# Performance work log

Measured on AMD Instinct MI355X. Metric: run time of the kernel, lower is better.

## Reference

```python
import jax, jax.numpy as jnp
import numpy as np

B, H_IN, W_IN = 8192, 26, 26

def _conv(x, w, b):
    # NCHW conv, stride 1, padding 1 (as in OffConv2d: padding hardcoded to 1)
    y = jax.lax.conv_general_dilated(x, w, (1, 1), [(1, 1), (1, 1)],
                                     dimension_numbers=('NCHW', 'OIHW', 'NCHW'))
    return y + b[None, :, None, None]

def _grid_sample_bilinear_zeros(img, gx, gy):
    # img: (N,H,W), gx/gy: (N,H,W) normalized coords; matches torch grid_sample
    # mode='bilinear', padding_mode='zeros', align_corners=False
    N, H, W = img.shape
    ix = ((gx + 1.0) * W - 1.0) * 0.5
    iy = ((gy + 1.0) * H - 1.0) * 0.5
    x0 = jnp.floor(ix); y0 = jnp.floor(iy)
    x1 = x0 + 1.0;      y1 = y0 + 1.0
    wx1 = ix - x0; wx0 = 1.0 - wx1
    wy1 = iy - y0; wy0 = 1.0 - wy1
    bi = jnp.arange(N)[:, None, None]
    def gather(yy, xx):
        valid = (xx >= 0) & (xx < W) & (yy >= 0) & (yy < H)
        v = img[bi,
                jnp.clip(yy, 0, H - 1).astype(jnp.int32),
                jnp.clip(xx, 0, W - 1).astype(jnp.int32)]
        return jnp.where(valid, v, 0.0)
    return (gather(y0, x0) * wy0 * wx0 + gather(y0, x1) * wy0 * wx1 +
            gather(y1, x0) * wy1 * wx0 + gather(y1, x1) * wy1 * wx1)

def _off_conv(x, ws, bs, wx, bx, wy, by):
    s  = _conv(x, ws, bs)   # score  (B,C,H,W)
    gx = _conv(x, wx, bx)   # offset_x -> grid x coord
    gy = _conv(x, wy, by)   # offset_y -> grid y coord
    b, c, h, w = s.shape
    out = _grid_sample_bilinear_zeros(s.reshape(b * c, h, w),
                                      gx.reshape(b * c, h, w),
                                      gy.reshape(b * c, h, w))
    return out.reshape(b, c, h, w)

def _maxpool2(x):
    return jax.lax.reduce_window(x, -jnp.inf, jax.lax.max,
                                 (1, 1, 2, 2), (1, 1, 2, 2), 'VALID')

def setup_inputs() -> dict:
    key = jax.random.key(0)
    ks = jax.random.split(key, 20)
    r = lambda k, shp, s: (jax.random.normal(k, shp, dtype=jnp.float32) * s)
    inp = {
        'x':   r(ks[0], (B, H_IN, W_IN), 1.0),
        'w1s': r(ks[1], (6, 1, 5, 5), 0.2),  'b1s': r(ks[2], (6,), 0.1),
        'w1x': r(ks[3], (6, 1, 5, 5), 0.2),  'b1x': r(ks[4], (6,), 0.1),
        'w1y': r(ks[5], (6, 1, 5, 5), 0.2),  'b1y': r(ks[6], (6,), 0.1),
        'w2s': r(ks[7], (16, 6, 5, 5), 0.1), 'b2s': r(ks[8], (16,), 0.1),
        'w2x': r(ks[9], (16, 6, 5, 5), 0.1), 'b2x': r(ks[10], (16,), 0.1),
        'w2y': r(ks[11], (16, 6, 5, 5), 0.1),'b2y': r(ks[12], (16,), 0.1),
        'wf1': r(ks[13], (120, 400), 0.05),  'bf1': r(ks[14], (120,), 0.05),
        'wf2': r(ks[15], (84, 120), 0.05),   'bf2': r(ks[16], (84,), 0.05),
        'wf3': r(ks[17], (10, 84), 0.05),    'bf3': r(ks[18], (10,), 0.05),
    }
    return inp

def reference(x, w1s, b1s, w1x, b1x, w1y, b1y,
              w2s, b2s, w2x, b2x, w2y, b2y,
              wf1, bf1, wf2, bf2, wf3, bf3):
    h = x[:, None, :, :]                                   # (B,1,26,26)
    h = _maxpool2(jax.nn.relu(_off_conv(h, w1s, b1s, w1x, b1x, w1y, b1y)))  # (B,6,12,12)
    h = _maxpool2(jax.nn.relu(_off_conv(h, w2s, b2s, w2x, b2x, w2y, b2y)))  # (B,16,5,5)
    h = h.reshape(-1, 16 * 5 * 5)
    h = jax.nn.relu(h @ wf1.T + bf1)
    h = jax.nn.relu(h @ wf2.T + bf2)
    h = h @ wf3.T + bf3
    return jax.nn.softmax(h, axis=1)
```

## Files before the change

### kernel.cpp

```cpp
#include <hip/hip_runtime.h>
#include <math.h>

#define TPB 256

typedef float v2f __attribute__((ext_vector_type(2)));

__device__ __forceinline__ void pk_lo(v2f& acc, v2f ap, v2f w) {
    asm("v_pk_fma_f32 %0, %1, %2, %0 op_sel:[0,0,0] op_sel_hi:[0,1,1]"
        : "+v"(acc) : "v"(ap), "v"(w));
}
__device__ __forceinline__ void pk_hi(v2f& acc, v2f ap, v2f w) {
    asm("v_pk_fma_f32 %0, %1, %2, %0 op_sel:[1,0,0] op_sel_hi:[1,1,1]"
        : "+v"(acc) : "v"(ap), "v"(w));
}

#define OFF_WA_SX 0
#define OFF_WA_YY 300
#define OFF_WB_SX 464
#define OFF_WB_YY 5264
#define OFF_WF1T  7664
#define OFF_WF2T  55664
#define OFF_WF3T  65744
#define OFF_H1    66592
#define OFF_H2    7144480
#define WS_FLOATS 10421280ull
#define REQ_WS_BYTES (WS_FLOATS * 4ull)

__device__ __forceinline__ float bilin_zero(const float* __restrict__ img, int N,
                                            float gx, float gy) {
    float fx = (gx + 1.0f) * (0.5f * (float)N) - 0.5f;
    float fy = (gy + 1.0f) * (0.5f * (float)N) - 0.5f;
    float x0 = floorf(fx), y0 = floorf(fy);
    float wx1 = fx - x0, wy1 = fy - y0;
    float wx0 = 1.0f - wx1, wy0 = 1.0f - wy1;
    float x1 = x0 + 1.0f, y1 = y0 + 1.0f;
    float Nm1 = (float)(N - 1);
    int xi0 = (int)fminf(fmaxf(x0, 0.0f), Nm1);
    int yi0 = (int)fminf(fmaxf(y0, 0.0f), Nm1);
    int xi1 = (int)fminf(fmaxf(x1, 0.0f), Nm1);
    int yi1 = (int)fminf(fmaxf(y1, 0.0f), Nm1);
    bool vx0 = (x0 >= 0.0f) && (x0 < (float)N);
    bool vx1 = (x1 >= 0.0f) && (x1 < (float)N);
    bool vy0 = (y0 >= 0.0f) && (y0 < (float)N);
    bool vy1 = (y1 >= 0.0f) && (y1 < (float)N);
    float v00 = (vy0 && vx0) ? img[yi0 * N + xi0] : 0.0f;
    float v01 = (vy0 && vx1) ? img[yi0 * N + xi1] : 0.0f;
    float v10 = (vy1 && vx0) ? img[yi1 * N + xi0] : 0.0f;
    float v11 = (vy1 && vx1) ? img[yi1 * N + xi1] : 0.0f;
    return v00 * wy0 * wx0 + v01 * wy0 * wx1 + v10 * wy1 * wx0 + v11 * wy1 * wx1;
}

__global__ __launch_bounds__(TPB) void lenet_prep(
    const float* __restrict__ w1s, const float* __restrict__ w1x, const float* __restrict__ w1y,
    const float* __restrict__ w2s, const float* __restrict__ w2x, const float* __restrict__ w2y,
    const float* __restrict__ wf1, const float* __restrict__ wf2, const float* __restrict__ wf3,
    float* __restrict__ wsf)
{
    int g = blockIdx.x * TPB + threadIdx.x;
    int stride = gridDim.x * TPB;
    for (int i = g; i < 75; i += stride) {
        int cp = i / 25, t = i % 25;
        int cA = (2 * cp) * 25 + t, cB = (2 * cp + 1) * 25 + t;
        float* p = wsf + OFF_WA_SX + i * 4;
        p[0] = w1s[cA]; p[1] = w1x[cA]; p[2] = w1s[cB]; p[3] = w1x[cB];
        wsf[OFF_WA_YY + i * 2 + 0] = w1y[cA];
        wsf[OFF_WA_YY + i * 2 + 1] = w1y[cB];
    }
    for (int e = g; e < 1200; e += stride) {
        int cp = e / 150, rem = e % 150;
        int iA = cp * 150 + rem, iB = (cp + 8) * 150 + rem;
        float* pp = wsf + OFF_WB_SX + e * 4;
        pp[0] = w2s[iA]; pp[1] = w2s[iB]; pp[2] = w2x[iA]; pp[3] = w2x[iB];
        wsf[OFF_WB_YY + e * 2 + 0] = w2y[iA];
        wsf[OFF_WB_YY + e * 2 + 1] = w2y[iB];
    }
    for (int i = g; i < 48000; i += stride) { int k = i / 120, o = i % 120; wsf[OFF_WF1T + i] = wf1[o * 400 + k]; }
    for (int i = g; i < 10080; i += stride) { int k = i / 84,  o = i % 84;  wsf[OFF_WF2T + i] = wf2[o * 120 + k]; }
    for (int i = g; i < 840;   i += stride) { int k = i / 10,  o = i % 10;  wsf[OFF_WF3T + i] = wf3[o * 84 + k]; }
}

__global__ __launch_bounds__(TPB) void lenetA(
    const float* __restrict__ x, const float* __restrict__ wsf,
    const float* __restrict__ b1s, const float* __restrict__ b1x, const float* __restrict__ b1y,
    float* __restrict__ h1)
{
    __shared__ __align__(16) float xs_p[784];
    __shared__ __align__(16) float smap1[3456];

    const int tid = threadIdx.x, b = blockIdx.x;
    const float* xp = x + b * 676;
    for (int i = tid; i < 784; i += TPB) {
        int r = i / 28, c = i % 28;
        float v = 0.0f;
        if (r >= 1 && r <= 26 && c >= 1 && c <= 26) v = xp[(r - 1) * 26 + (c - 1)];
        xs_p[i] = v;
    }
    __syncthreads();

    const float4* wsx = (const float4*)(wsf + OFF_WA_SX);
    const v2f*    wyy = (const v2f*)   (wsf + OFF_WA_YY);

    float gxa[2][2][2][2], gya[2][2][2][2];
    #pragma unroll
    for (int it = 0; it < 2; ++it) {
        int idx = tid + it * TPB;
        if (idx < 432) {
            int cp = idx / 144, p = idx % 144;
            int py = p / 12, px = p % 12;
            v2f aw[6][3];
            #pragma unroll
            for (int r = 0; r < 6; ++r) {
                const v2f* rp = (const v2f*)&xs_p[(2 * py + r) * 28 + 2 * px];
                aw[r][0] = rp[0]; aw[r][1] = rp[1]; aw[r][2] = rp[2];
            }
            int c0 = 2 * cp, c1 = 2 * cp + 1;
            v2f a0[2][2], a1[2][2], ay[2][2];
            {
                v2f i0 = {b1s[c0], b1x[c0]};
                v2f i1 = {b1s[c1], b1x[c1]};
                v2f iy = {b1y[c0], b1y[c1]};
                #pragma unroll
                for (int dy = 0; dy < 2; ++dy)
                    #pragma unroll
                    for (int dx = 0; dx < 2; ++dx) { a0[dy][dx] = i0; a1[dy][dx] = i1; ay[dy][dx] = iy; }
            }
            const float4* wp  = wsx + cp * 25;
            const v2f*    wyp = wyy + cp * 25;
            #pragma unroll
            for (int ky = 0; ky < 5; ++ky)
                #pragma unroll
                for (int kx = 0; kx < 5; ++kx) {
                    float4 w4 = wp[ky * 5 + kx];
                    v2f wA = {w4.x, w4.y};
                    v2f wB = {w4.z, w4.w};
                    v2f wy = wyp[ky * 5 + kx];
                    #pragma unroll
                    for (int dy = 0; dy < 2; ++dy)
                        #pragma unroll
                        for (int dx = 0; dx < 2; ++dx) {
                            int rr = ky + dy, cc = kx + dx;
                            v2f ap = aw[rr][cc >> 1];
                            if ((cc & 1) == 0) {
                                pk_lo(a0[dy][dx], ap, wA);
                                pk_lo(a1[dy][dx], ap, wB);
                                pk_lo(ay[dy][dx], ap, wy);
                            } else {
                                pk_hi(a0[dy][dx], ap, wA);
                                pk_hi(a1[dy][dx], ap, wB);
                                pk_hi(ay[dy][dx], ap, wy);
                            }
                        }
                }
            {
                v2f r00 = {a0[0][0].x, a0[0][1].x};
                v2f r01 = {a0[1][0].x, a0[1][1].x};
                v2f r10 = {a1[0][0].x, a1[0][1].x};
                v2f r11 = {a1[1][0].x, a1[1][1].x};
                *(v2f*)&smap1[c0 * 576 + (2 * py) * 24 + 2 * px]     = r00;
                *(v2f*)&smap1[c0 * 576 + (2 * py + 1) * 24 + 2 * px] = r01;
                *(v2f*)&smap1[c1 * 576 + (2 * py) * 24 + 2 * px]     = r10;
                *(v2f*)&smap1[c1 * 576 + (2 * py + 1) * 24 + 2 * px] = r11;
            }
            #pragma unroll
            for (int dy = 0; dy < 2; ++dy)
                #pragma unroll
                for (int dx = 0; dx < 2; ++dx) {
                    gxa[it][0][dy][dx] = a0[dy][dx].y;  gya[it][0][dy][dx] = ay[dy][dx].x;
                    gxa[it][1][dy][dx] = a1[dy][dx].y;  gya[it][1][dy][dx] = ay[dy][dx].y;
                }
        }
    }
    __syncthreads();

    #pragma unroll
    for (int it = 0; it < 2; ++it) {
        int idx = tid + it * TPB;
        if (idx < 432) {
            int cp = idx / 144, p = idx % 144;
            #pragma unroll
            for (int ch = 0; ch < 2; ++ch) {
                int c = 2 * cp + ch;
                const float* smc = &smap1[c * 576];
                float mx = 0.0f;
                #pragma unroll
                for (int dy = 0; dy < 2; ++dy)
                    #pragma unroll
                    for (int dx = 0; dx < 2; ++dx)
                        mx = fmaxf(mx, bilin_zero(smc, 24, gxa[it][ch][dy][dx], gya[it][ch][dy][dx]));
                h1[b * 864 + c * 144 + p] = mx;
            }
        }
    }
}

__global__ __launch_bounds__(TPB, 5) void lenetB(
    const float* __restrict__ h1, const float* __restrict__ wsf,
    const float* __restrict__ b2s, const float* __restrict__ b2x, const float* __restrict__ b2y,
    float* __restrict__ h2)
{
    __shared__ __align__(16) float h1p[2][1176];
    __shared__ __align__(16) float wsm[4][2][2][100];

    const int tid = threadIdx.x, b = blockIdx.x;

    for (int i = tid; i < 2352; i += TPB) {
        int im = (i >= 1176) ? 1 : 0;
        int k = i - im * 1176;
        int ch = k / 196, pp = k % 196;
        int r = pp / 14, c = pp % 14;
        float v = 0.0f;
        if (r >= 1 && r <= 12 && c >= 1 && c <= 12)
            v = h1[(size_t)(2 * b + im) * 864 + ch * 144 + (r - 1) * 12 + (c - 1)];
        h1p[im][k] = v;
    }
    __syncthreads();

    const int lane = tid & 63;
    const int wvu  = __builtin_amdgcn_readfirstlane(tid >> 6);
    const int img  = lane >> 5;
    const int p    = lane & 31;
    const bool act = (p < 25);
    const int py = p / 5, px = p % 5;

    const float4* wsx = (const float4*)(wsf + OFF_WB_SX);
    const v2f*    wyy = (const v2f*)   (wsf + OFF_WB_YY);
    float* smw = &wsm[wvu][img][0][0];

    #pragma unroll
    for (int rep = 0; rep < 2; ++rep) {
        const int cp = wvu + 4 * rep;
        if (rep) {
            asm volatile("s_waitcnt lgkmcnt(0)" ::: "memory");
            __builtin_amdgcn_sched_barrier(0);
        }
        v2f as[2][2], ax[2][2], ay[2][2];
        if (act) {
            {
                v2f is = {b2s[cp], b2s[cp + 8]};
                v2f ix = {b2x[cp], b2x[cp + 8]};
                v2f iy = {b2y[cp], b2y[cp + 8]};
                #pragma unroll
                for (int dy = 0; dy < 2; ++dy)
                    #pragma unroll
                    for (int dx = 0; dx < 2; ++dx) { as[dy][dx] = is; ax[dy][dx] = ix; ay[dy][dx] = iy; }
            }
            #pragma unroll
            for (int i = 0; i < 6; ++i) {
                v2f aw[6][3];
                #pragma unroll
                for (int r = 0; r < 6; ++r) {
                    const v2f* rp = (const v2f*)&h1p[img][i * 196 + (2 * py + r) * 14 + 2 * px];
                    aw[r][0] = rp[0]; aw[r][1] = rp[1]; aw[r][2] = rp[2];
                }
                const float4* wt  = wsx + (cp * 6 + i) * 25;
                const v2f*    wyt = wyy + (cp * 6 + i) * 25;
                #pragma unroll
                for (int ky = 0; ky < 5; ++ky)
                    #pragma unroll
                    for (int kx = 0; kx < 5; ++kx) {
                        float4 w4 = wt[ky * 5 + kx];
                        v2f ws = {w4.x, w4.y};
                        v2f wx = {w4.z, w4.w};
                        v2f wy = wyt[ky * 5 + kx];
                        #pragma unroll
                        for (int dy = 0; dy < 2; ++dy)
                            #pragma unroll
                            for (int dx = 0; dx < 2; ++dx) {
                                int cc = kx + dx;
                                v2f ap = aw[ky + dy][cc >> 1];
                                if ((cc & 1) == 0) {
                                    pk_lo(as[dy][dx], ap, ws);
                                    pk_lo(ax[dy][dx], ap, wx);
                                    pk_lo(ay[dy][dx], ap, wy);
                                } else {
                                    pk_hi(as[dy][dx], ap, ws);
                                    pk_hi(ax[dy][dx], ap, wx);
                                    pk_hi(ay[dy][dx], ap, wy);
                                }
                            }
                    }
            }
            {
                int base0 = (2 * py) * 10 + 2 * px;
                int base1 = base0 + 10;
                *(v2f*)&smw[base0]       = (v2f){as[0][0].x, as[0][1].x};
                *(v2f*)&smw[base1]       = (v2f){as[1][0].x, as[1][1].x};
                *(v2f*)&smw[100 + base0] = (v2f){as[0][0].y, as[0][1].y};
                *(v2f*)&smw[100 + base1] = (v2f){as[1][0].y, as[1][1].y};
            }
        }
        asm volatile("s_waitcnt lgkmcnt(0)" ::: "memory");
        __builtin_amdgcn_sched_barrier(0);
        if (act) {
            #pragma unroll
            for (int slot = 0; slot < 2; ++slot) {
                int c = cp + slot * 8;
                const float* smc = &smw[slot * 100];
                float mx = 0.0f;
                #pragma unroll
                for (int dy = 0; dy < 2; ++dy)
                    #pragma unroll
                    for (int dx = 0; dx < 2; ++dx) {
                        float gx = slot ? ax[dy][dx].y : ax[dy][dx].x;
                        float gy = slot ? ay[dy][dx].y : ay[dy][dx].x;
                        mx = fmaxf(mx, bilin_zero(smc, 10, gx, gy));
                    }
                h2[(size_t)(2 * b + img) * 400 + c * 25 + p] = mx;
            }
        }
    }
}

__global__ __launch_bounds__(TPB) void lenetC(
    const float* __restrict__ h2, const float* __restrict__ wsf,
    const float* __restrict__ bf1, const float* __restrict__ bf2, const float* __restrict__ bf3,
    float* __restrict__ out)
{
    __shared__ __align__(16) float h2s[4][4][400];
    __shared__ float f1s[4][4][120];
    __shared__ float f2s[4][4][84];
    __shared__ float f3s[4][4][10];

    const int tid = threadIdx.x;
    const int w = tid >> 6, lane = tid & 63;
    const int img0 = blockIdx.x * 16 + w * 4;

    for (int j = 0; j < 4; ++j) {
        float4*       dst = (float4*)&h2s[w][j][0];
        const float4* src = (const float4*)&h2[(img0 + j) * 400];
        for (int k = lane; k < 100; k += 64) dst[k] = src[k];
    }
    __syncthreads();

    {
        const float* wf1T = wsf + OFF_WF1T;
        float acc1[4] = {0, 0, 0, 0}, acc2[4] = {0, 0, 0, 0};
        for (int k = 0; k < 400; ++k) {
            float wa = wf1T[k * 120 + lane];
            float wb = (lane < 56) ? wf1T[k * 120 + 64 + lane] : 0.0f;
            #pragma unroll
            for (int j = 0; j < 4; ++j) {
                float hv = h2s[w][j][k];
                acc1[j] = fmaf(hv, wa, acc1[j]);
                acc2[j] = fmaf(hv, wb, acc2[j]);
            }
        }
        float bb1 = bf1[lane];
        float bb2 = (lane < 56) ? bf1[64 + lane] : 0.0f;
        #pragma unroll
        for (int j = 0; j < 4; ++j) {
            f1s[w][j][lane] = fmaxf(acc1[j] + bb1, 0.0f);
            if (lane < 56) f1s[w][j][64 + lane] = fmaxf(acc2[j] + bb2, 0.0f);
        }
    }
    __syncthreads();

    {
        const float* wf2T = wsf + OFF_WF2T;
        float acc1[4], acc2[4];
        float bb1 = bf2[lane];
        float bb2 = (lane < 20) ? bf2[64 + lane] : 0.0f;
        #pragma unroll
        for (int j = 0; j < 4; ++j) { acc1[j] = bb1; acc2[j] = bb2; }
        for (int k = 0; k < 120; ++k) {
            float wa = wf2T[k * 84 + lane];
            float wb = (lane < 20) ? wf2T[k * 84 + 64 + lane] : 0.0f;
            #pragma unroll
            for (int j = 0; j < 4; ++j) {
                float hv = f1s[w][j][k];
                acc1[j] = fmaf(hv, wa, acc1[j]);
                acc2[j] = fmaf(hv, wb, acc2[j]);
            }
        }
        #pragma unroll
        for (int j = 0; j < 4; ++j) {
            f2s[w][j][lane] = fmaxf(acc1[j], 0.0f);
            if (lane < 20) f2s[w][j][64 + lane] = fmaxf(acc2[j], 0.0f);
        }
    }
    __syncthreads();

    if (lane < 10) {
        const float* wf3T = wsf + OFF_WF3T;
        float acc[4];
        float bb = bf3[lane];
        #pragma unroll
        for (int j = 0; j < 4; ++j) acc[j] = bb;
        for (int k = 0; k < 84; ++k) {
            float wv = wf3T[k * 10 + lane];
            #pragma unroll
            for (int j = 0; j < 4; ++j) acc[j] = fmaf(f2s[w][j][k], wv, acc[j]);
        }
        #pragma unroll
        for (int j = 0; j < 4; ++j) f3s[w][j][lane] = acc[j];
    }
    __syncthreads();

    if (lane < 40) {
        int j = lane / 10, c = lane % 10;
        float m = f3s[w][j][0];
        #pragma unroll
        for (int q = 1; q < 10; ++q) m = fmaxf(m, f3s[w][j][q]);
        float ssum = 0.0f;
        #pragma unroll
        for (int q = 0; q < 10; ++q) ssum += expf(f3s[w][j][q] - m);
        out[(img0 + j) * 10 + c] = expf(f3s[w][j][c] - m) / ssum;
    }
}

__global__ __launch_bounds__(TPB, 2) void lenet_off_fused(
    const float* __restrict__ x,
    const float* __restrict__ w1s, const float* __restrict__ b1s,
    const float* __restrict__ w1x, const float* __restrict__ b1x,
    const float* __restrict__ w1y, const float* __restrict__ b1y,
    const float* __restrict__ w2s, const float* __restrict__ b2s,
    const float* __restrict__ w2x, const float* __restrict__ b2x,
    const float* __restrict__ w2y, const float* __restrict__ b2y,
    const float* __restrict__ wf1, const float* __restrict__ bf1,
    const float* __restrict__ wf2, const float* __restrict__ bf2,
    const float* __restrict__ wf3, const float* __restrict__ bf3,
    float* __restrict__ out)
{
    __shared__ __align__(16) float  xs_p[784];
    __shared__ float4 w1i[150];
    __shared__ float4 b1i[6];
    __shared__ float4 w2i[2400];
    __shared__ float4 b2i[16];
    __shared__ __align__(16) float  smap1[3456];
    __shared__ __align__(16) float  h1p[1176];
    __shared__ __align__(16) float  smap2[1600];
    __shared__ __align__(16) float  h2[400];
    __shared__ __align__(16) float  f1[120];
    __shared__ __align__(16) float  f2[84];
    __shared__ float  f3[10];

    const int tid = threadIdx.x;
    const int b   = blockIdx.x;

    const float* xp = x + b * 676;
    for (int i = tid; i < 784; i += TPB) {
        int r = i / 28, c = i % 28;
        float v = 0.0f;
        if (r >= 1 && r <= 26 && c >= 1 && c <= 26) v = xp[(r - 1) * 26 + (c - 1)];
        xs_p[i] = v;
    }
    for (int i = tid; i < 150; i += TPB)
        w1i[i] = make_float4(w1s[i], w1x[i], w1y[i], 0.0f);
    if (tid < 6)  b1i[tid] = make_float4(b1s[tid], b1x[tid], b1y[tid], 0.0f);
    for (int i = tid; i < 2400; i += TPB)
        w2i[i] = make_float4(w2s[i], w2x[i], w2y[i], 0.0f);
    if (tid < 16) b2i[tid] = make_float4(b2s[tid], b2x[tid], b2y[tid], 0.0f);
    for (int i = tid; i < 1176; i += TPB) h1p[i] = 0.0f;
    __syncthreads();

    float gxr[4][2][2], gyr[4][2][2];
    #pragma unroll
    for (int it = 0; it < 4; ++it) {
        int idx = tid + it * TPB;
        if (idx < 864) {
            int c = idx / 144, p = idx % 144;
            int py = p / 12, px = p % 12;
            float a[6][6];
            #pragma unroll
            for (int r = 0; r < 6; ++r) {
                const float2* rp = (const float2*)&xs_p[(2 * py + r) * 28 + 2 * px];
                float2 v0 = rp[0], v1 = rp[1], v2 = rp[2];
                a[r][0] = v0.x; a[r][1] = v0.y; a[r][2] = v1.x;
                a[r][3] = v1.y; a[r][4] = v2.x; a[r][5] = v2.y;
            }
            float4 bb = b1i[c];
            float s[2][2], agx[2][2], agy[2][2];
            #pragma unroll
            for (int dy = 0; dy < 2; ++dy)
                #pragma unroll
                for (int dx = 0; dx < 2; ++dx) { s[dy][dx] = bb.x; agx[dy][dx] = bb.y; agy[dy][dx] = bb.z; }
            #pragma unroll
            for (int ky = 0; ky < 5; ++ky)
                #pragma unroll
                for (int kx = 0; kx < 5; ++kx) {
                    float4 w = w1i[c * 25 + ky * 5 + kx];
                    #pragma unroll
                    for (int dy = 0; dy < 2; ++dy)
                        #pragma unroll
                        for (int dx = 0; dx < 2; ++dx) {
                            float v = a[ky + dy][kx + dx];
                            s[dy][dx]   = fmaf(v, w.x, s[dy][dx]);
                            agx[dy][dx] = fmaf(v, w.y, agx[dy][dx]);
                            agy[dy][dx] = fmaf(v, w.z, agy[dy][dx]);
                        }
                }
            float* sm = &smap1[c * 576 + (2 * py) * 24 + 2 * px];
            sm[0] = s[0][0]; sm[1] = s[0][1]; sm[24] = s[1][0]; sm[25] = s[1][1];
            #pragma unroll
            for (int dy = 0; dy < 2; ++dy)
                #pragma unroll
                for (int dx = 0; dx < 2; ++dx) { gxr[it][dy][dx] = agx[dy][dx]; gyr[it][dy][dx] = agy[dy][dx]; }
        }
    }
    __syncthreads();

    #pragma unroll
    for (int it = 0; it < 4; ++it) {
        int idx = tid + it * TPB;
        if (idx < 864) {
            int c = idx / 144, p = idx % 144;
            int py = p / 12, px = p % 12;
            const float* smc = &smap1[c * 576];
            float mx = 0.0f;
            #pragma unroll
            for (int dy = 0; dy < 2; ++dy)
                #pragma unroll
                for (int dx = 0; dx < 2; ++dx)
                    mx = fmaxf(mx, bilin_zero(smc, 24, gxr[it][dy][dx], gyr[it][dy][dx]));
            h1p[c * 196 + (py + 1) * 14 + (px + 1)] = mx;
        }
    }
    __syncthreads();

    float gxr2[2][2][2], gyr2[2][2][2];
    #pragma unroll
    for (int it = 0; it < 2; ++it) {
        int idx = tid + it * TPB;
        if (idx < 400) {
            int c = idx / 25, p = idx % 25;
            int py = p / 5, px = p % 5;
            float4 bb = b2i[c];
            float s[2][2], agx[2][2], agy[2][2];
            #pragma unroll
            for (int dy = 0; dy < 2; ++dy)
                #pragma unroll
                for (int dx = 0; dx < 2; ++dx) { s[dy][dx] = bb.x; agx[dy][dx] = bb.y; agy[dy][dx] = bb.z; }
            for (int i = 0; i < 6; ++i) {
                float a[6][6];
                #pragma unroll
                for (int r = 0; r < 6; ++r) {
                    const float2* rp = (const float2*)&h1p[i * 196 + (2 * py + r) * 14 + 2 * px];
                    float2 v0 = rp[0], v1 = rp[1], v2 = rp[2];
                    a[r][0] = v0.x; a[r][1] = v0.y; a[r][2] = v1.x;
                    a[r][3] = v1.y; a[r][4] = v2.x; a[r][5] = v2.y;
                }
                const float4* wc = &w2i[c * 150 + i * 25];
                #pragma unroll
                for (int ky = 0; ky < 5; ++ky)
                    #pragma unroll
                    for (int kx = 0; kx < 5; ++kx) {
                        float4 w = wc[ky * 5 + kx];
                        #pragma unroll
                        for (int dy = 0; dy < 2; ++dy)
                            #pragma unroll
                            for (int dx = 0; dx < 2; ++dx) {
                                float v = a[ky + dy][kx + dx];
                                s[dy][dx]   = fmaf(v, w.x, s[dy][dx]);
                                agx[dy][dx] = fmaf(v, w.y, agx[dy][dx]);
                                agy[dy][dx] = fmaf(v, w.z, agy[dy][dx]);
                            }
                    }
            }
            float* sm = &smap2[c * 100 + (2 * py) * 10 + 2 * px];
            sm[0] = s[0][0]; sm[1] = s[0][1]; sm[10] = s[1][0]; sm[11] = s[1][1];
            #pragma unroll
            for (int dy = 0; dy < 2; ++dy)
                #pragma unroll
                for (int dx = 0; dx < 2; ++dx) { gxr2[it][dy][dx] = agx[dy][dx]; gyr2[it][dy][dx] = agy[dy][dx]; }
        }
    }
    __syncthreads();

    #pragma unroll
    for (int it = 0; it < 2; ++it) {
        int idx = tid + it * TPB;
        if (idx < 400) {
            int c = idx / 25, p = idx % 25;
            int py = p / 5, px = p % 5;
            const float* smc = &smap2[c * 100];
            float mx = 0.0f;
            #pragma unroll
            for (int dy = 0; dy < 2; ++dy)
                #pragma unroll
                for (int dx = 0; dx < 2; ++dx)
                    mx = fmaxf(mx, bilin_zero(smc, 10, gxr2[it][dy][dx], gyr2[it][dy][dx]));
            h2[c * 25 + py * 5 + px] = mx;
        }
    }
    __syncthreads();

    if (tid < 240) {
        int o = tid >> 1, h = tid & 1;
        const float4* wrow = (const float4*)(wf1 + o * 400 + h * 200);
        const float4* hh   = (const float4*)&h2[h * 200];
        float acc = 0.0f;
        for (int k = 0; k < 50; ++k) {
            float4 w = wrow[k]; float4 v = hh[k];
            acc = fmaf(w.x, v.x, acc); acc = fmaf(w.y, v.y, acc);
            acc = fmaf(w.z, v.z, acc); acc = fmaf(w.w, v.w, acc);
        }
        acc += __shfl_xor(acc, 1);
        if (h == 0) f1[o] = fmaxf(acc + bf1[o], 0.0f);
    }
    __syncthreads();

    if (tid < 84) {
        const float4* wrow = (const float4*)(wf2 + tid * 120);
        const float4* hh   = (const float4*)f1;
        float acc = bf2[tid];
        for (int k = 0; k < 30; ++k) {
            float4 w = wrow[k]; float4 v = hh[k];
            acc = fmaf(w.x, v.x, acc); acc = fmaf(w.y, v.y, acc);
            acc = fmaf(w.z, v.z, acc); acc = fmaf(w.w, v.w, acc);
        }
        f2[tid] = fmaxf(acc, 0.0f);
    }
    __syncthreads();

    if (tid < 10) {
        const float4* wrow = (const float4*)(wf3 + tid * 84);
        const float4* hh   = (const float4*)f2;
        float acc = bf3[tid];
        for (int k = 0; k < 21; ++k) {
            float4 w = wrow[k]; float4 v = hh[k];
            acc = fmaf(w.x, v.x, acc); acc = fmaf(w.y, v.y, acc);
            acc = fmaf(w.z, v.z, acc); acc = fmaf(w.w, v.w, acc);
        }
        f3[tid] = acc;
    }
    __syncthreads();

    if (tid < 10) {
        float m = f3[0];
        #pragma unroll
        for (int j = 1; j < 10; ++j) m = fmaxf(m, f3[j]);
        float ssum = 0.0f;
        #pragma unroll
        for (int j = 0; j < 10; ++j) ssum += expf(f3[j] - m);
        out[b * 10 + tid] = expf(f3[tid] - m) / ssum;
    }
}

extern "C" void kernel_launch(void* const* d_in, const int* in_sizes, int n_in,
                              void* d_out, int out_size, void* d_ws, size_t ws_size,
                              hipStream_t stream) {
    const float* x   = (const float*)d_in[0];
    const float* w1s = (const float*)d_in[1];
    const float* b1s = (const float*)d_in[2];
    const float* w1x = (const float*)d_in[3];
    const float* b1x = (const float*)d_in[4];
    const float* w1y = (const float*)d_in[5];
    const float* b1y = (const float*)d_in[6];
    const float* w2s = (const float*)d_in[7];
    const float* b2s = (const float*)d_in[8];
    const float* w2x = (const float*)d_in[9];
    const float* b2x = (const float*)d_in[10];
    const float* w2y = (const float*)d_in[11];
    const float* b2y = (const float*)d_in[12];
    const float* wf1 = (const float*)d_in[13];
    const float* bf1 = (const float*)d_in[14];
    const float* wf2 = (const float*)d_in[15];
    const float* bf2 = (const float*)d_in[16];
    const float* wf3 = (const float*)d_in[17];
    const float* bf3 = (const float*)d_in[18];
    float* out = (float*)d_out;

    if (ws_size >= REQ_WS_BYTES) {
        float* wsf = (float*)d_ws;
        lenet_prep<<<64, TPB, 0, stream>>>(w1s, w1x, w1y, w2s, w2x, w2y,
                                           wf1, wf2, wf3, wsf);
        lenetA<<<8192, TPB, 0, stream>>>(x, wsf, b1s, b1x, b1y, wsf + OFF_H1);
        lenetB<<<4096, TPB, 0, stream>>>(wsf + OFF_H1, wsf, b2s, b2x, b2y, wsf + OFF_H2);
        lenetC<<<512, TPB, 0, stream>>>(wsf + OFF_H2, wsf, bf1, bf2, bf3, out);
    } else {
        lenet_off_fused<<<8192, TPB, 0, stream>>>(
            x, w1s, b1s, w1x, b1x, w1y, b1y,
            w2s, b2s, w2x, b2x, w2y, b2y,
            wf1, bf1, wf2, bf2, wf3, bf3, out);
    }
}
```

Baseline: 336.0 us.

## Restructure conv1 kernel: two images per block, wave-private score maps, no block barrier

The layer-1 kernel now handles two images per 384-thread block. Each wave owns one (image, channel-pair) and loops over three passes of 48 lanes, writing its score maps into a wave-private shared buffer. This lets the block-wide barrier before bilinear sampling be replaced by a wave-local lgkmcnt wait. Input rows are streamed through two rotating register rows instead of a 6x3 window, to cut register pressure. In exchange, a quarter of each wave's lanes sit idle and shared memory per block grows, which may lower occupancy.

```diff
diff --git a/kernel.cpp b/kernel.cpp
--- a/kernel.cpp
+++ b/kernel.cpp
@@ -2,6 +2,7 @@
 #include <math.h>
 
 #define TPB 256
+#define TPBA 384
 
 typedef float v2f __attribute__((ext_vector_type(2)));
 
@@ -79,41 +80,48 @@
     for (int i = g; i < 840;   i += stride) { int k = i / 10,  o = i % 10;  wsf[OFF_WF3T + i] = wf3[o * 84 + k]; }
 }
 
-__global__ __launch_bounds__(TPB) void lenetA(
+__global__ __launch_bounds__(TPBA) void lenetA(
     const float* __restrict__ x, const float* __restrict__ wsf,
     const float* __restrict__ b1s, const float* __restrict__ b1x, const float* __restrict__ b1y,
     float* __restrict__ h1)
 {
-    __shared__ __align__(16) float xs_p[784];
-    __shared__ __align__(16) float smap1[3456];
+    __shared__ __align__(16) float xs_p[2][784];
+    __shared__ __align__(16) float wsm[6][1152];
 
     const int tid = threadIdx.x, b = blockIdx.x;
-    const float* xp = x + b * 676;
-    for (int i = tid; i < 784; i += TPB) {
-        int r = i / 28, c = i % 28;
+
+    for (int i = tid; i < 1568; i += TPBA) {
+        int im = (i >= 784) ? 1 : 0;
+        int k = i - im * 784;
+        int r = k / 28, c = k % 28;
         float v = 0.0f;
-        if (r >= 1 && r <= 26 && c >= 1 && c <= 26) v = xp[(r - 1) * 26 + (c - 1)];
-        xs_p[i] = v;
-    }
-    __syncthreads();
+        if (r >= 1 && r <= 26 && c >= 1 && c <= 26)
+            v = x[(size_t)(2 * b + im) * 676 + (r - 1) * 26 + (c - 1)];
+        xs_p[im][k] = v;
+    }
+    __syncthreads();
+
+    const int lane = tid & 63;
+    const int wvu  = __builtin_amdgcn_readfirstlane(tid >> 6);
+    const int img  = wvu / 3;
+    const int cp   = wvu % 3;
+    const int c0   = 2 * cp, c1 = 2 * cp + 1;
+    const bool act = (lane < 48);
 
     const float4* wsx = (const float4*)(wsf + OFF_WA_SX);
     const v2f*    wyy = (const v2f*)   (wsf + OFF_WA_YY);
-
-    float gxa[2][2][2][2], gya[2][2][2][2];
+    const float4* wp  = wsx + cp * 25;
+    const v2f*    wyp = wyy + cp * 25;
+    float* smw = &wsm[wvu][0];
+
+    float gxa[3][2][2][2], gya[3][2][2][2];
+
     #pragma unroll
-    for (int it = 0; it < 2; ++it) {
-        int idx = tid + it * TPB;
-        if (idx < 432) {
-            int cp = idx / 144, p = idx % 144;
-            int py = p / 12, px = p % 12;
-            v2f aw[6][3];
-            #pragma unroll
-            for (int r = 0; r < 6; ++r) {
-                const v2f* rp = (const v2f*)&xs_p[(2 * py + r) * 28 + 2 * px];
-                aw[r][0] = rp[0]; aw[r][1] = rp[1]; aw[r][2] = rp[2];
-            }
-            int c0 = 2 * cp, c1 = 2 * cp + 1;
+    for (int pass = 0; pass < 3; ++pass) {
+        int p = pass * 48 + lane;
+        int py = p / 12, px = p % 12;
+        if (act) {
+            const float* xsb = &xs_p[img][(2 * py) * 28 + 2 * px];
             v2f a0[2][2], a1[2][2], ay[2][2];
             {
                 v2f i0 = {b1s[c0], b1x[c0]};
@@ -124,10 +132,12 @@
                     #pragma unroll
                     for (int dx = 0; dx < 2; ++dx) { a0[dy][dx] = i0; a1[dy][dx] = i1; ay[dy][dx] = iy; }
             }
-            const float4* wp  = wsx + cp * 25;
-            const v2f*    wyp = wyy + cp * 25;
-            #pragma unroll
-            for (int ky = 0; ky < 5; ++ky)
+            v2f rA[3], rB[3];
+            auto loadrow = [&](v2f* dst, int r) {
+                const v2f* rp = (const v2f*)&xsb[r * 28];
+                dst[0] = rp[0]; dst[1] = rp[1]; dst[2] = rp[2];
+            };
+            auto dorow = [&](const v2f* rlo, const v2f* rhi, int ky) {
                 #pragma unroll
                 for (int kx = 0; kx < 5; ++kx) {
                     float4 w4 = wp[ky * 5 + kx];
@@ -135,11 +145,12 @@
                     v2f wB = {w4.z, w4.w};
                     v2f wy = wyp[ky * 5 + kx];
                     #pragma unroll
-                    for (int dy = 0; dy < 2; ++dy)
+                    for (int dy = 0; dy < 2; ++dy) {
+                        const v2f* row = dy ? rhi : rlo;
                         #pragma unroll
                         for (int dx = 0; dx < 2; ++dx) {
-                            int rr = ky + dy, cc = kx + dx;
-                            v2f ap = aw[rr][cc >> 1];
+                            int cc = kx + dx;
+                            v2f ap = row[cc >> 1];
                             if ((cc & 1) == 0) {
                                 pk_lo(a0[dy][dx], ap, wA);
                                 pk_lo(a1[dy][dx], ap, wB);
@@ -150,44 +161,50 @@
                                 pk_hi(ay[dy][dx], ap, wy);
                             }
                         }
+                    }
                 }
+            };
+            loadrow(rA, 0); loadrow(rB, 1); dorow(rA, rB, 0);
+            loadrow(rA, 2);                 dorow(rB, rA, 1);
+            loadrow(rB, 3);                 dorow(rA, rB, 2);
+            loadrow(rA, 4);                 dorow(rB, rA, 3);
+            loadrow(rB, 5);                 dorow(rA, rB, 4);
+
             {
-                v2f r00 = {a0[0][0].x, a0[0][1].x};
-                v2f r01 = {a0[1][0].x, a0[1][1].x};
-                v2f r10 = {a1[0][0].x, a1[0][1].x};
-                v2f r11 = {a1[1][0].x, a1[1][1].x};
-                *(v2f*)&smap1[c0 * 576 + (2 * py) * 24 + 2 * px]     = r00;
-                *(v2f*)&smap1[c0 * 576 + (2 * py + 1) * 24 + 2 * px] = r01;
-                *(v2f*)&smap1[c1 * 576 + (2 * py) * 24 + 2 * px]     = r10;
-                *(v2f*)&smap1[c1 * 576 + (2 * py + 1) * 24 + 2 * px] = r11;
+                int base0 = (2 * py) * 24 + 2 * px;
+                int base1 = base0 + 24;
+                *(v2f*)&smw[base0]       = (v2f){a0[0][0].x, a0[0][1].x};
+                *(v2f*)&smw[base1]       = (v2f){a0[1][0].x, a0[1][1].x};
+                *(v2f*)&smw[576 + base0] = (v2f){a1[0][0].x, a1[0][1].x};
+                *(v2f*)&smw[576 + base1] = (v2f){a1[1][0].x, a1[1][1].x};
             }
             #pragma unroll
             for (int dy = 0; dy < 2; ++dy)
                 #pragma unroll
                 for (int dx = 0; dx < 2; ++dx) {
-                    gxa[it][0][dy][dx] = a0[dy][dx].y;  gya[it][0][dy][dx] = ay[dy][dx].x;
-                    gxa[it][1][dy][dx] = a1[dy][dx].y;  gya[it][1][dy][dx] = ay[dy][dx].y;
+                    gxa[pass][0][dy][dx] = a0[dy][dx].y;  gya[pass][0][dy][dx] = ay[dy][dx].x;
+                    gxa[pass][1][dy][dx] = a1[dy][dx].y;  gya[pass][1][dy][dx] = ay[dy][dx].y;
                 }
         }
     }
-    __syncthreads();
+
+    asm volatile("s_waitcnt lgkmcnt(0)" ::: "memory");
+    __builtin_amdgcn_sched_barrier(0);
 
     #pragma unroll
-    for (int it = 0; it < 2; ++it) {
-        int idx = tid + it * TPB;
-        if (idx < 432) {
-            int cp = idx / 144, p = idx % 144;
+    for (int pass = 0; pass < 3; ++pass) {
+        int p = pass * 48 + lane;
+        if (act) {
             #pragma unroll
             for (int ch = 0; ch < 2; ++ch) {
-                int c = 2 * cp + ch;
-                const float* smc = &smap1[c * 576];
+                const float* smc = &smw[ch * 576];
                 float mx = 0.0f;
                 #pragma unroll
                 for (int dy = 0; dy < 2; ++dy)
                     #pragma unroll
                     for (int dx = 0; dx < 2; ++dx)
-                        mx = fmaxf(mx, bilin_zero(smc, 24, gxa[it][ch][dy][dx], gya[it][ch][dy][dx]));
-                h1[b * 864 + c * 144 + p] = mx;
+                        mx = fmaxf(mx, bilin_zero(smc, 24, gxa[pass][ch][dy][dx], gya[pass][ch][dy][dx]));
+                h1[(size_t)(2 * b + img) * 864 + (2 * cp + ch) * 144 + p] = mx;
             }
         }
     }
@@ -664,7 +681,7 @@
         float* wsf = (float*)d_ws;
         lenet_prep<<<64, TPB, 0, stream>>>(w1s, w1x, w1y, w2s, w2x, w2y,
                                            wf1, wf2, wf3, wsf);
-        lenetA<<<8192, TPB, 0, stream>>>(x, wsf, b1s, b1x, b1y, wsf + OFF_H1);
+        lenetA<<<4096, TPBA, 0, stream>>>(x, wsf, b1s, b1x, b1y, wsf + OFF_H1);
         lenetB<<<4096, TPB, 0, stream>>>(wsf + OFF_H1, wsf, b2s, b2x, b2y, wsf + OFF_H2);
         lenetC<<<512, TPB, 0, stream>>>(wsf + OFF_H2, wsf, bf1, bf2, bf3, out);
     } else {
```

New measurement: 365.4 us. 1.09x slower.

## Widen lenetA and lenetC blocks, one work item per thread, weights in LDS

Applied to the files above, without the earlier changes.

lenetA now launches 448 threads so each of the 432 conv/grid-sample work items gets its own thread, replacing the two-iteration loop over 256 threads. Its conv1 s/x weights and biases are staged in shared memory rather than read from global memory per thread. lenetC moves to 512 threads with 8 waves of 2 images each instead of 4 waves of 4 images, which doubles the waves per block. This increases parallelism and shortens per-thread serial work, at the cost of more threads per block, which may limit occupancy, and of wf1/wf2 weight loads now being shared across fewer images per wave.

```diff
diff --git a/kernel.cpp b/kernel.cpp
--- a/kernel.cpp
+++ b/kernel.cpp
@@ -2,6 +2,8 @@
 #include <math.h>
 
 #define TPB 256
+#define TPBA 448
+#define TPBC 512
 
 typedef float v2f __attribute__((ext_vector_type(2)));
 
@@ -79,116 +81,117 @@
     for (int i = g; i < 840;   i += stride) { int k = i / 10,  o = i % 10;  wsf[OFF_WF3T + i] = wf3[o * 84 + k]; }
 }
 
-__global__ __launch_bounds__(TPB) void lenetA(
+__global__ __launch_bounds__(TPBA) void lenetA(
     const float* __restrict__ x, const float* __restrict__ wsf,
     const float* __restrict__ b1s, const float* __restrict__ b1x, const float* __restrict__ b1y,
     float* __restrict__ h1)
 {
     __shared__ __align__(16) float xs_p[784];
+    __shared__ float4 w1i[150];
+    __shared__ float4 b1w[3];
+    __shared__ v2f    b1yw[3];
     __shared__ __align__(16) float smap1[3456];
 
     const int tid = threadIdx.x, b = blockIdx.x;
     const float* xp = x + b * 676;
-    for (int i = tid; i < 784; i += TPB) {
+    for (int i = tid; i < 784; i += TPBA) {
         int r = i / 28, c = i % 28;
         float v = 0.0f;
         if (r >= 1 && r <= 26 && c >= 1 && c <= 26) v = xp[(r - 1) * 26 + (c - 1)];
         xs_p[i] = v;
     }
-    __syncthreads();
-
-    const float4* wsx = (const float4*)(wsf + OFF_WA_SX);
-    const v2f*    wyy = (const v2f*)   (wsf + OFF_WA_YY);
-
-    float gxa[2][2][2][2], gya[2][2][2][2];
-    #pragma unroll
-    for (int it = 0; it < 2; ++it) {
-        int idx = tid + it * TPB;
-        if (idx < 432) {
-            int cp = idx / 144, p = idx % 144;
-            int py = p / 12, px = p % 12;
-            v2f aw[6][3];
-            #pragma unroll
-            for (int r = 0; r < 6; ++r) {
-                const v2f* rp = (const v2f*)&xs_p[(2 * py + r) * 28 + 2 * px];
-                aw[r][0] = rp[0]; aw[r][1] = rp[1]; aw[r][2] = rp[2];
-            }
-            int c0 = 2 * cp, c1 = 2 * cp + 1;
-            v2f a0[2][2], a1[2][2], ay[2][2];
-            {
-                v2f i0 = {b1s[c0], b1x[c0]};
-                v2f i1 = {b1s[c1], b1x[c1]};
-                v2f iy = {b1y[c0], b1y[c1]};
+    if (tid < 150) w1i[tid] = ((const float4*)(wsf + OFF_WA_SX))[tid];
+    if (tid < 3) {
+        b1w[tid]  = make_float4(b1s[2 * tid], b1x[2 * tid], b1s[2 * tid + 1], b1x[2 * tid + 1]);
+        b1yw[tid] = (v2f){b1y[2 * tid], b1y[2 * tid + 1]};
+    }
+    __syncthreads();
+
+    const v2f* wyy = (const v2f*)(wsf + OFF_WA_YY);
+
+    const int cp = tid / 144, p = tid % 144;
+    const int py = p / 12, px = p % 12;
+    const bool act = (tid < 432);
+
+    float gxa[2][2][2], gya[2][2][2];
+    if (act) {
+        v2f aw[6][3];
+        #pragma unroll
+        for (int r = 0; r < 6; ++r) {
+            const v2f* rp = (const v2f*)&xs_p[(2 * py + r) * 28 + 2 * px];
+            aw[r][0] = rp[0]; aw[r][1] = rp[1]; aw[r][2] = rp[2];
+        }
+        int c0 = 2 * cp, c1 = 2 * cp + 1;
+        v2f a0[2][2], a1[2][2], ay[2][2];
+        {
+            float4 bb = b1w[cp];
+            v2f i0 = {bb.x, bb.y};
+            v2f i1 = {bb.z, bb.w};
+            v2f iy = b1yw[cp];
+            #pragma unroll
+            for (int dy = 0; dy < 2; ++dy)
+                #pragma unroll
+                for (int dx = 0; dx < 2; ++dx) { a0[dy][dx] = i0; a1[dy][dx] = i1; ay[dy][dx] = iy; }
+        }
+        const float4* wp  = &w1i[cp * 25];
+        const v2f*    wyp = wyy + cp * 25;
+        #pragma unroll
+        for (int ky = 0; ky < 5; ++ky)
+            #pragma unroll
+            for (int kx = 0; kx < 5; ++kx) {
+                float4 w4 = wp[ky * 5 + kx];
+                v2f wA = {w4.x, w4.y};
+                v2f wB = {w4.z, w4.w};
+                v2f wy = wyp[ky * 5 + kx];
                 #pragma unroll
                 for (int dy = 0; dy < 2; ++dy)
                     #pragma unroll
-                    for (int dx = 0; dx < 2; ++dx) { a0[dy][dx] = i0; a1[dy][dx] = i1; ay[dy][dx] = iy; }
-            }
-            const float4* wp  = wsx + cp * 25;
-            const v2f*    wyp = wyy + cp * 25;
-            #pragma unroll
-            for (int ky = 0; ky < 5; ++ky)
-                #pragma unroll
-                for (int kx = 0; kx < 5; ++kx) {
-                    float4 w4 = wp[ky * 5 + kx];
-                    v2f wA = {w4.x, w4.y};
-                    v2f wB = {w4.z, w4.w};
-                    v2f wy = wyp[ky * 5 + kx];
-                    #pragma unroll
-                    for (int dy = 0; dy < 2; ++dy)
-                        #pragma unroll
-                        for (int dx = 0; dx < 2; ++dx) {
-                            int rr = ky + dy, cc = kx + dx;
-                            v2f ap = aw[rr][cc >> 1];
-                            if ((cc & 1) == 0) {
-                                pk_lo(a0[dy][dx], ap, wA);
-                                pk_lo(a1[dy][dx], ap, wB);
-                                pk_lo(ay[dy][dx], ap, wy);
-                            } else {
-                                pk_hi(a0[dy][dx], ap, wA);
-                                pk_hi(a1[dy][dx], ap, wB);
-                                pk_hi(ay[dy][dx], ap, wy);
-                            }
+                    for (int dx = 0; dx < 2; ++dx) {
+                        int cc = kx + dx;
+                        v2f ap = aw[ky + dy][cc >> 1];
+                        if ((cc & 1) == 0) {
+                            pk_lo(a0[dy][dx], ap, wA);
+                            pk_lo(a1[dy][dx], ap, wB);
+                            pk_lo(ay[dy][dx], ap, wy);
+                        } else {
+                            pk_hi(a0[dy][dx], ap, wA);
+                            pk_hi(a1[dy][dx], ap, wB);
+                            pk_hi(ay[dy][dx], ap, wy);
                         }
-                }
-            {
-                v2f r00 = {a0[0][0].x, a0[0][1].x};
-                v2f r01 = {a0[1][0].x, a0[1][1].x};
-                v2f r10 = {a1[0][0].x, a1[0][1].x};
-                v2f r11 = {a1[1][0].x, a1[1][1].x};
-                *(v2f*)&smap1[c0 * 576 + (2 * py) * 24 + 2 * px]     = r00;
-                *(v2f*)&smap1[c0 * 576 + (2 * py + 1) * 24 + 2 * px] = r01;
-                *(v2f*)&smap1[c1 * 576 + (2 * py) * 24 + 2 * px]     = r10;
-                *(v2f*)&smap1[c1 * 576 + (2 * py + 1) * 24 + 2 * px] = r11;
-            }
-            #pragma unroll
-            for (int dy = 0; dy < 2; ++dy)
-                #pragma unroll
-                for (int dx = 0; dx < 2; ++dx) {
-                    gxa[it][0][dy][dx] = a0[dy][dx].y;  gya[it][0][dy][dx] = ay[dy][dx].x;
-                    gxa[it][1][dy][dx] = a1[dy][dx].y;  gya[it][1][dy][dx] = ay[dy][dx].y;
-                }
-        }
-    }
-    __syncthreads();
-
-    #pragma unroll
-    for (int it = 0; it < 2; ++it) {
-        int idx = tid + it * TPB;
-        if (idx < 432) {
-            int cp = idx / 144, p = idx % 144;
-            #pragma unroll
-            for (int ch = 0; ch < 2; ++ch) {
-                int c = 2 * cp + ch;
-                const float* smc = &smap1[c * 576];
-                float mx = 0.0f;
-                #pragma unroll
-                for (int dy = 0; dy < 2; ++dy)
-                    #pragma unroll
-                    for (int dx = 0; dx < 2; ++dx)
-                        mx = fmaxf(mx, bilin_zero(smc, 24, gxa[it][ch][dy][dx], gya[it][ch][dy][dx]));
-                h1[b * 864 + c * 144 + p] = mx;
-            }
+                    }
+            }
+        {
+            v2f r00 = {a0[0][0].x, a0[0][1].x};
+            v2f r01 = {a0[1][0].x, a0[1][1].x};
+            v2f r10 = {a1[0][0].x, a1[0][1].x};
+            v2f r11 = {a1[1][0].x, a1[1][1].x};
+            *(v2f*)&smap1[c0 * 576 + (2 * py) * 24 + 2 * px]     = r00;
+            *(v2f*)&smap1[c0 * 576 + (2 * py + 1) * 24 + 2 * px] = r01;
+            *(v2f*)&smap1[c1 * 576 + (2 * py) * 24 + 2 * px]     = r10;
+            *(v2f*)&smap1[c1 * 576 + (2 * py + 1) * 24 + 2 * px] = r11;
+        }
+        #pragma unroll
+        for (int dy = 0; dy < 2; ++dy)
+            #pragma unroll
+            for (int dx = 0; dx < 2; ++dx) {
+                gxa[0][dy][dx] = a0[dy][dx].y;  gya[0][dy][dx] = ay[dy][dx].x;
+                gxa[1][dy][dx] = a1[dy][dx].y;  gya[1][dy][dx] = ay[dy][dx].y;
+            }
+    }
+    __syncthreads();
+
+    if (act) {
+        #pragma unroll
+        for (int ch = 0; ch < 2; ++ch) {
+            int c = 2 * cp + ch;
+            const float* smc = &smap1[c * 576];
+            float mx = 0.0f;
+            #pragma unroll
+            for (int dy = 0; dy < 2; ++dy)
+                #pragma unroll
+                for (int dx = 0; dx < 2; ++dx)
+                    mx = fmaxf(mx, bilin_zero(smc, 24, gxa[ch][dy][dx], gya[ch][dy][dx]));
+            h1[(size_t)b * 864 + c * 144 + p] = mx;
         }
     }
 }
@@ -311,21 +314,21 @@
     }
 }
 
-__global__ __launch_bounds__(TPB) void lenetC(
+__global__ __launch_bounds__(TPBC) void lenetC(
     const float* __restrict__ h2, const float* __restrict__ wsf,
     const float* __restrict__ bf1, const float* __restrict__ bf2, const float* __restrict__ bf3,
     float* __restrict__ out)
 {
-    __shared__ __align__(16) float h2s[4][4][400];
-    __shared__ float f1s[4][4][120];
-    __shared__ float f2s[4][4][84];
-    __shared__ float f3s[4][4][10];
+    __shared__ __align__(16) float h2s[8][2][400];
+    __shared__ float f1s[8][2][120];
+    __shared__ float f2s[8][2][84];
+    __shared__ float f3s[8][2][10];
 
     const int tid = threadIdx.x;
     const int w = tid >> 6, lane = tid & 63;
-    const int img0 = blockIdx.x * 16 + w * 4;
-
-    for (int j = 0; j < 4; ++j) {
+    const int img0 = blockIdx.x * 16 + w * 2;
+
+    for (int j = 0; j < 2; ++j) {
         float4*       dst = (float4*)&h2s[w][j][0];
         const float4* src = (const float4*)&h2[(img0 + j) * 400];
         for (int k = lane; k < 100; k += 64) dst[k] = src[k];
@@ -334,12 +337,12 @@
 
     {
         const float* wf1T = wsf + OFF_WF1T;
-        float acc1[4] = {0, 0, 0, 0}, acc2[4] = {0, 0, 0, 0};
+        float acc1[2] = {0, 0}, acc2[2] = {0, 0};
         for (int k = 0; k < 400; ++k) {
             float wa = wf1T[k * 120 + lane];
             float wb = (lane < 56) ? wf1T[k * 120 + 64 + lane] : 0.0f;
             #pragma unroll
-            for (int j = 0; j < 4; ++j) {
+            for (int j = 0; j < 2; ++j) {
                 float hv = h2s[w][j][k];
                 acc1[j] = fmaf(hv, wa, acc1[j]);
                 acc2[j] = fmaf(hv, wb, acc2[j]);
@@ -348,7 +351,7 @@
         float bb1 = bf1[lane];
         float bb2 = (lane < 56) ? bf1[64 + lane] : 0.0f;
         #pragma unroll
-        for (int j = 0; j < 4; ++j) {
+        for (int j = 0; j < 2; ++j) {
             f1s[w][j][lane] = fmaxf(acc1[j] + bb1, 0.0f);
             if (lane < 56) f1s[w][j][64 + lane] = fmaxf(acc2[j] + bb2, 0.0f);
         }
@@ -357,23 +360,23 @@
 
     {
         const float* wf2T = wsf + OFF_WF2T;
-        float acc1[4], acc2[4];
+        float acc1[2], acc2[2];
         float bb1 = bf2[lane];
         float bb2 = (lane < 20) ? bf2[64 + lane] : 0.0f;
         #pragma unroll
-        for (int j = 0; j < 4; ++j) { acc1[j] = bb1; acc2[j] = bb2; }
+        for (int j = 0; j < 2; ++j) { acc1[j] = bb1; acc2[j] = bb2; }
         for (int k = 0; k < 120; ++k) {
             float wa = wf2T[k * 84 + lane];
             float wb = (lane < 20) ? wf2T[k * 84 + 64 + lane] : 0.0f;
             #pragma unroll
-            for (int j = 0; j < 4; ++j) {
+            for (int j = 0; j < 2; ++j) {
                 float hv = f1s[w][j][k];
                 acc1[j] = fmaf(hv, wa, acc1[j]);
                 acc2[j] = fmaf(hv, wb, acc2[j]);
             }
         }
         #pragma unroll
-        for (int j = 0; j < 4; ++j) {
+        for (int j = 0; j < 2; ++j) {
             f2s[w][j][lane] = fmaxf(acc1[j], 0.0f);
             if (lane < 20) f2s[w][j][64 + lane] = fmaxf(acc2[j], 0.0f);
         }
@@ -382,21 +385,21 @@
 
     if (lane < 10) {
         const float* wf3T = wsf + OFF_WF3T;
-        float acc[4];
+        float acc[2];
         float bb = bf3[lane];
         #pragma unroll
-        for (int j = 0; j < 4; ++j) acc[j] = bb;
+        for (int j = 0; j < 2; ++j) acc[j] = bb;
         for (int k = 0; k < 84; ++k) {
             float wv = wf3T[k * 10 + lane];
             #pragma unroll
-            for (int j = 0; j < 4; ++j) acc[j] = fmaf(f2s[w][j][k], wv, acc[j]);
-        }
-        #pragma unroll
-        for (int j = 0; j < 4; ++j) f3s[w][j][lane] = acc[j];
-    }
-    __syncthreads();
-
-    if (lane < 40) {
+            for (int j = 0; j < 2; ++j) acc[j] = fmaf(f2s[w][j][k], wv, acc[j]);
+        }
+        #pragma unroll
+        for (int j = 0; j < 2; ++j) f3s[w][j][lane] = acc[j];
+    }
+    __syncthreads();
+
+    if (lane < 20) {
         int j = lane / 10, c = lane % 10;
         float m = f3s[w][j][0];
         #pragma unroll
@@ -664,9 +667,9 @@
         float* wsf = (float*)d_ws;
         lenet_prep<<<64, TPB, 0, stream>>>(w1s, w1x, w1y, w2s, w2x, w2y,
                                            wf1, wf2, wf3, wsf);
-        lenetA<<<8192, TPB, 0, stream>>>(x, wsf, b1s, b1x, b1y, wsf + OFF_H1);
+        lenetA<<<8192, TPBA, 0, stream>>>(x, wsf, b1s, b1x, b1y, wsf + OFF_H1);
         lenetB<<<4096, TPB, 0, stream>>>(wsf + OFF_H1, wsf, b2s, b2x, b2y, wsf + OFF_H2);
-        lenetC<<<512, TPB, 0, stream>>>(wsf + OFF_H2, wsf, bf1, bf2, bf3, out);
+        lenetC<<<512, TPBC, 0, stream>>>(wsf + OFF_H2, wsf, bf1, bf2, bf3, out);
     } else {
         lenet_off_fused<<<8192, TPB, 0, stream>>>(
             x, w1s, b1s, w1x, b1x, w1y, b1y,
```

New measurement: 326.3 us. -2.9%, faster.
